# Kernel tuning notes

Hardware: AMD Instinct MI355X
Metric: run time of the kernel (lower is better)

The kernel has to match this reference:

```python
import jax, jax.numpy as jnp
import numpy as np

EMBED_DIM = 1024
BATCH, SEQ = 4, 2048


def setup_inputs() -> dict:
    key = jax.random.key(0)
    k1, k2 = jax.random.split(key)
    hidden_states = jax.random.normal(k1, (BATCH, SEQ, EMBED_DIM), dtype=jnp.float32)
    # fused QKV projection weight (Linear(embed_dim, 3*embed_dim, bias=False)),
    # stored as [E, 3E] so y = x @ W
    W_qkv = jax.random.normal(k2, (EMBED_DIM, 3 * EMBED_DIM), dtype=jnp.float32) * (1.0 / np.sqrt(EMBED_DIM))
    return {"hidden_states": hidden_states, "W_qkv": W_qkv}


def reference(hidden_states, W_qkv):
    E = hidden_states.shape[-1]
    scale = 1.0 / np.sqrt(E)
    qkv = jnp.einsum('bse,ef->bsf', hidden_states, W_qkv)  # [B,S,3E]
    q, k, v = jnp.split(qkv, 3, axis=-1)                   # each [B,S,E]
    # scores = q @ (k^T * scale); softmax over keys
    scores = jnp.einsum('bqe,bke->bqk', q, k) * scale      # [B,S,S]
    w = jax.nn.softmax(scores, axis=-1)
    return jnp.einsum('bqk,bke->bqe', w, v)                # [B,S,E]
```

## Files before the change

### kernel.cpp

```cpp
#include <hip/hip_runtime.h>

typedef __attribute__((ext_vector_type(8))) short short8;
typedef __attribute__((ext_vector_type(8))) unsigned short ushort8;
typedef __attribute__((ext_vector_type(4))) float f32x4;

__device__ __forceinline__ float bf2f(unsigned short u) {
  union { unsigned int u; float f; } c; c.u = ((unsigned int)u) << 16; return c.f;
}
__device__ __forceinline__ unsigned short f2bf(float f) {
  union { float f; unsigned int u; } c; c.f = f;
  unsigned int x = c.u;
  return (unsigned short)((x + 0x7FFFu + ((x >> 16) & 1u)) >> 16);
}

#define GLD_LDS16(g, l)                                                        \
  __builtin_amdgcn_global_load_lds(                                            \
      (const __attribute__((address_space(1))) void*)(g),                      \
      (__attribute__((address_space(3))) void*)(l), 16, 0, 0)

__global__ __launch_bounds__(256) void prep_kernel(
    const float* __restrict__ X, unsigned short* __restrict__ Xb,
    const float* __restrict__ W, unsigned short* __restrict__ Wt) {
  const int t = threadIdx.x;
  if (blockIdx.x < 4096) {
    long i = ((long)blockIdx.x * 256 + t) * 8;
    float4 a = *(const float4*)(X + i);
    float4 b = *(const float4*)(X + i + 4);
    ushort8 o;
    o[0] = f2bf(a.x); o[1] = f2bf(a.y); o[2] = f2bf(a.z); o[3] = f2bf(a.w);
    o[4] = f2bf(b.x); o[5] = f2bf(b.y); o[6] = f2bf(b.z); o[7] = f2bf(b.w);
    *(ushort8*)(Xb + i) = o;
  } else {
    const int bid = blockIdx.x - 4096;
    const int f0 = (bid % 48) * 64;
    const int e0 = (bid / 48) * 64;
    __shared__ unsigned short tile[64][65];
    const int cg = (t & 15) * 4;
    const int r = t >> 4;
#pragma unroll
    for (int i = 0; i < 4; ++i) {
      int e = r + i * 16;
      float4 v = *(const float4*)(W + (long)(e0 + e) * 3072 + f0 + cg);
      tile[e][cg + 0] = f2bf(v.x);
      tile[e][cg + 1] = f2bf(v.y);
      tile[e][cg + 2] = f2bf(v.z);
      tile[e][cg + 3] = f2bf(v.w);
    }
    __syncthreads();
#pragma unroll
    for (int i = 0; i < 4; ++i) {
      int f = (t >> 4) + i * 16;
      int e = (t & 15) * 4;
      ushort4 o;
      o.x = tile[e + 0][f];
      o.y = tile[e + 1][f];
      o.z = tile[e + 2][f];
      o.w = tile[e + 3][f];
      *(ushort4*)(Wt + (long)(f0 + f) * 1024 + e0 + e) = o;
    }
  }
}

template <int MODE>
__device__ __forceinline__ void gemm_body(
    const unsigned short* __restrict__ A, const unsigned short* __restrict__ B,
    void* __restrict__ Cv, int K, int lda, int ldb, int ldc,
    long sA, long sB, long sC, float alpha, float* __restrict__ Lrow,
    unsigned short* __restrict__ Vt) {
  constexpr int BM = 128, BN = 128, BK = 64;
  __shared__ __align__(16) unsigned short smem[BM * BK + BN * BK];
  unsigned short* As = smem;
  unsigned short* Bs = smem + BM * BK;

  const int t = threadIdx.x;
  const int lane = t & 63;
  const int wave = t >> 6;
  const int quad = lane >> 4;
  const int mrow = lane & 15;
  const int wm = wave >> 1, wn = wave & 1;

  const int bx = blockIdx.x, by = blockIdx.y;
  const int rowA0 = by * BM;
  const int rowB0 = bx * BN;
  const int b = blockIdx.z;
  const unsigned short* Ab = A + (long)b * sA;
  const unsigned short* Bb = B + (long)b * sB;

  f32x4 acc[4][4];
#pragma unroll
  for (int i = 0; i < 4; ++i)
#pragma unroll
    for (int j = 0; j < 4; ++j) {
      f32x4 z = {0.f, 0.f, 0.f, 0.f};
      acc[i][j] = z;
    }

  const int rbase = wave * 32 + (lane >> 3);
  const int c2 = lane & 7;

  for (int kt = 0; kt < K; kt += BK) {
#pragma unroll
    for (int j = 0; j < 4; ++j) {
      int r = rbase + j * 8;
      int c = c2 ^ (r & 7);
      GLD_LDS16(Ab + (long)(rowA0 + r) * lda + kt + c * 8, As + (wave * 4 + j) * 512);
      GLD_LDS16(Bb + (long)(rowB0 + r) * ldb + kt + c * 8, Bs + (wave * 4 + j) * 512);
    }
    __syncthreads();
#pragma unroll
    for (int ks = 0; ks < 2; ++ks) {
      short8 af[4], bfr[4];
#pragma unroll
      for (int i = 0; i < 4; ++i) {
        int rA = wm * 64 + i * 16 + mrow;
        int cc = ks * 4 + quad;
        af[i] = *(const short8*)(As + (rA * 8 + (cc ^ (rA & 7))) * 8);
        int rB = wn * 64 + i * 16 + mrow;
        bfr[i] = *(const short8*)(Bs + (rB * 8 + (cc ^ (rB & 7))) * 8);
      }
#pragma unroll
      for (int mt = 0; mt < 4; ++mt)
#pragma unroll
        for (int nt = 0; nt < 4; ++nt)
          acc[mt][nt] = __builtin_amdgcn_mfma_f32_16x16x32_bf16(
              af[mt], bfr[nt], acc[mt][nt], 0, 0, 0);
    }
    __syncthreads();
  }

  const int m_base = rowA0 + wm * 64;
  const int n_base = rowB0 + wn * 64;
  const long cb = (long)b * sC;

  if constexpr (MODE == 0) {
    if (bx < 16) {
#pragma unroll
      for (int mt = 0; mt < 4; ++mt)
#pragma unroll
        for (int nt = 0; nt < 4; ++nt)
#pragma unroll
          for (int i = 0; i < 4; ++i) {
            int row = m_base + mt * 16 + quad * 4 + i;
            int col = n_base + nt * 16 + mrow;
            ((unsigned short*)Cv)[cb + (long)row * ldc + col] = f2bf(acc[mt][nt][i]);
          }
    } else {
#pragma unroll
      for (int mt = 0; mt < 4; ++mt)
#pragma unroll
        for (int nt = 0; nt < 4; ++nt)
#pragma unroll
          for (int i = 0; i < 4; ++i) {
            int r = wm * 64 + mt * 16 + quad * 4 + i;
            int cL = wn * 64 + nt * 16 + mrow;
            int swz = ((cL & 7) << 4) ^ (((cL >> 3) & 3) << 3);
            smem[cL * 128 + (r ^ swz)] = f2bf(acc[mt][nt][i]);
          }
      __syncthreads();
      const int batch = by >> 4;
      const int s_base = (by & 15) * 128;
      const int e_base = (bx - 16) * 128;
      unsigned short* VtB = Vt + (long)batch * 1024 * 2048;
#pragma unroll
      for (int rnd = 0; rnd < 8; ++rnd) {
        int e = (t >> 4) + rnd * 16;
        int s = (t & 15) * 8;
        int swz = ((e & 7) << 4) ^ (((e >> 3) & 3) << 3);
        ushort8 v = *(const ushort8*)(smem + e * 128 + (s ^ swz));
        *(ushort8*)(VtB + (long)(e_base + e) * 2048 + s_base + s) = v;
      }
    }
  } else if constexpr (MODE == 1) {
    float p[4][4];
#pragma unroll
    for (int mt = 0; mt < 4; ++mt)
#pragma unroll
      for (int i = 0; i < 4; ++i) p[mt][i] = 0.f;
#pragma unroll
    for (int mt = 0; mt < 4; ++mt)
#pragma unroll
      for (int nt = 0; nt < 4; ++nt)
#pragma unroll
        for (int i = 0; i < 4; ++i) {
          int row = m_base + mt * 16 + quad * 4 + i;
          int col = n_base + nt * 16 + mrow;
          float e = __expf(acc[mt][nt][i] * alpha);
          ((unsigned short*)Cv)[cb + (long)row * ldc + col] = f2bf(e);
          p[mt][i] += e;
        }
#pragma unroll
    for (int off = 1; off < 16; off <<= 1)
#pragma unroll
      for (int mt = 0; mt < 4; ++mt)
#pragma unroll
        for (int i = 0; i < 4; ++i)
          p[mt][i] += __shfl_xor(p[mt][i], off, 64);
    if (mrow == 0) {
#pragma unroll
      for (int mt = 0; mt < 4; ++mt)
#pragma unroll
        for (int i = 0; i < 4; ++i) {
          int row = m_base + mt * 16 + quad * 4 + i;
          atomicAdd(&Lrow[b * 2048 + row], p[mt][i]);
        }
    }
  } else {
#pragma unroll
    for (int mt = 0; mt < 4; ++mt)
#pragma unroll
      for (int i = 0; i < 4; ++i) {
        int row = m_base + mt * 16 + quad * 4 + i;
        float inv = 1.0f / Lrow[b * 2048 + row];
#pragma unroll
        for (int nt = 0; nt < 4; ++nt) {
          int col = n_base + nt * 16 + mrow;
          ((float*)Cv)[cb + (long)row * ldc + col] = acc[mt][nt][i] * inv;
        }
      }
  }
}

__global__ __launch_bounds__(256, 2) void qkv_gemm_kernel(
    const unsigned short* __restrict__ A, const unsigned short* __restrict__ B,
    void* __restrict__ Cv, int K, int lda, int ldb, int ldc,
    long sA, long sB, long sC, float alpha, float* __restrict__ Lrow,
    unsigned short* __restrict__ Vt) {
  gemm_body<0>(A, B, Cv, K, lda, ldb, ldc, sA, sB, sC, alpha, Lrow, Vt);
}
__global__ __launch_bounds__(256, 2) void score_gemm_kernel(
    const unsigned short* __restrict__ A, const unsigned short* __restrict__ B,
    void* __restrict__ Cv, int K, int lda, int ldb, int ldc,
    long sA, long sB, long sC, float alpha, float* __restrict__ Lrow,
    unsigned short* __restrict__ Vt) {
  gemm_body<1>(A, B, Cv, K, lda, ldb, ldc, sA, sB, sC, alpha, Lrow, Vt);
}
__global__ __launch_bounds__(256, 2) void out_gemm_kernel(
    const unsigned short* __restrict__ A, const unsigned short* __restrict__ B,
    void* __restrict__ Cv, int K, int lda, int ldb, int ldc,
    long sA, long sB, long sC, float alpha, float* __restrict__ Lrow,
    unsigned short* __restrict__ Vt) {
  gemm_body<2>(A, B, Cv, K, lda, ldb, ldc, sA, sB, sC, alpha, Lrow, Vt);
}

extern "C" void kernel_launch(void* const* d_in, const int* in_sizes, int n_in,
                              void* d_out, int out_size, void* d_ws, size_t ws_size,
                              hipStream_t stream) {
  const float* X = (const float*)d_in[0];
  const float* W = (const float*)d_in[1];
  float* out = (float*)d_out;

  char* ws = (char*)d_ws;
  unsigned short* Xb  = (unsigned short*)(ws);
  unsigned short* Wtb = (unsigned short*)(ws + 16777216);
  unsigned short* QKV = (unsigned short*)(ws + 23068672);
  unsigned short* Vt  = (unsigned short*)(ws + 73400320);
  unsigned short* Sb  = (unsigned short*)(ws + 90177536);
  float* Lrow = (float*)(ws + 16777216);

  prep_kernel<<<4864, 256, 0, stream>>>(X, Xb, W, Wtb);

  qkv_gemm_kernel<<<dim3(24, 64, 1), 256, 0, stream>>>(
      Xb, Wtb, QKV, 1024, 1024, 1024, 3072, 0L, 0L, 0L, 1.0f, nullptr, Vt);

  hipMemsetAsync(Lrow, 0, 4 * 2048 * sizeof(float), stream);

  score_gemm_kernel<<<dim3(16, 16, 4), 256, 0, stream>>>(
      QKV, QKV + 1024, Sb, 1024, 3072, 3072, 2048,
      (long)2048 * 3072, (long)2048 * 3072, (long)2048 * 2048, 0.03125f, Lrow, nullptr);

  out_gemm_kernel<<<dim3(8, 16, 4), 256, 0, stream>>>(
      Sb, Vt, out, 2048, 2048, 2048, 1024,
      (long)2048 * 2048, (long)1024 * 2048, (long)2048 * 1024, 1.0f, Lrow, nullptr);
}
```

Baseline: 232.3 us.

## Split-K the output GEMM with atomics, fold memsets into prep, compact QK buffer

Splits the P·V output GEMM along K into two halves, doubling the grid to 1024 blocks, with partial results accumulated into the output by float atomicAdd. The output and the row-sum buffer are now zeroed by extra blocks in the prep kernel, which replaces the separate memset. The QKV projection now stores only Q and K, with a row stride of 2048, because V already goes to the transposed buffer. The V-transpose store to shared memory packs four bf16 values into one ushort4 write. The aim is better occupancy on the output GEMM and one fewer launch, at the cost of atomic traffic on the output and nondeterministic summation order.

```diff
diff --git a/kernel.cpp b/kernel.cpp
--- a/kernel.cpp
+++ b/kernel.cpp
@@ -20,7 +20,8 @@
 
 __global__ __launch_bounds__(256) void prep_kernel(
     const float* __restrict__ X, unsigned short* __restrict__ Xb,
-    const float* __restrict__ W, unsigned short* __restrict__ Wt) {
+    const float* __restrict__ W, unsigned short* __restrict__ Wt,
+    float* __restrict__ out, float* __restrict__ Lrow) {
   const int t = threadIdx.x;
   if (blockIdx.x < 4096) {
     long i = ((long)blockIdx.x * 256 + t) * 8;
@@ -30,7 +31,7 @@
     o[0] = f2bf(a.x); o[1] = f2bf(a.y); o[2] = f2bf(a.z); o[3] = f2bf(a.w);
     o[4] = f2bf(b.x); o[5] = f2bf(b.y); o[6] = f2bf(b.z); o[7] = f2bf(b.w);
     *(ushort8*)(Xb + i) = o;
-  } else {
+  } else if (blockIdx.x < 4864) {
     const int bid = blockIdx.x - 4096;
     const int f0 = (bid % 48) * 64;
     const int e0 = (bid / 48) * 64;
@@ -58,6 +59,15 @@
       o.w = tile[e + 3][f];
       *(ushort4*)(Wt + (long)(f0 + f) * 1024 + e0 + e) = o;
     }
+  } else if (blockIdx.x < 8960) {
+    long base = (long)(blockIdx.x - 4864) * 2048 + t * 8;
+    float4 z = {0.f, 0.f, 0.f, 0.f};
+    *(float4*)(out + base) = z;
+    *(float4*)(out + base + 4) = z;
+  } else {
+    float4 z = {0.f, 0.f, 0.f, 0.f};
+#pragma unroll
+    for (int j = 0; j < 8; ++j) *(float4*)(Lrow + (j * 256 + t) * 4) = z;
   }
 }
 
@@ -82,9 +92,16 @@
   const int bx = blockIdx.x, by = blockIdx.y;
   const int rowA0 = by * BM;
   const int rowB0 = bx * BN;
-  const int b = blockIdx.z;
-  const unsigned short* Ab = A + (long)b * sA;
-  const unsigned short* Bb = B + (long)b * sB;
+  int b, kbase;
+  if constexpr (MODE == 2) {
+    b = blockIdx.z >> 1;
+    kbase = (blockIdx.z & 1) * K;
+  } else {
+    b = blockIdx.z;
+    kbase = 0;
+  }
+  const unsigned short* Ab = A + (long)b * sA + kbase;
+  const unsigned short* Bb = B + (long)b * sB + kbase;
 
   f32x4 acc[4][4];
 #pragma unroll
@@ -148,14 +165,17 @@
 #pragma unroll
       for (int mt = 0; mt < 4; ++mt)
 #pragma unroll
-        for (int nt = 0; nt < 4; ++nt)
-#pragma unroll
-          for (int i = 0; i < 4; ++i) {
-            int r = wm * 64 + mt * 16 + quad * 4 + i;
-            int cL = wn * 64 + nt * 16 + mrow;
-            int swz = ((cL & 7) << 4) ^ (((cL >> 3) & 3) << 3);
-            smem[cL * 128 + (r ^ swz)] = f2bf(acc[mt][nt][i]);
-          }
+        for (int nt = 0; nt < 4; ++nt) {
+          int r4 = wm * 64 + mt * 16 + quad * 4;
+          int cL = wn * 64 + nt * 16 + mrow;
+          int swz = ((cL & 7) << 4) ^ (((cL >> 3) & 3) << 3);
+          ushort4 pk;
+          pk.x = f2bf(acc[mt][nt][0]);
+          pk.y = f2bf(acc[mt][nt][1]);
+          pk.z = f2bf(acc[mt][nt][2]);
+          pk.w = f2bf(acc[mt][nt][3]);
+          *(ushort4*)(smem + cL * 128 + (r4 ^ swz)) = pk;
+        }
       __syncthreads();
       const int batch = by >> 4;
       const int s_base = (by & 15) * 128;
@@ -214,7 +234,7 @@
 #pragma unroll
         for (int nt = 0; nt < 4; ++nt) {
           int col = n_base + nt * 16 + mrow;
-          ((float*)Cv)[cb + (long)row * ldc + col] = acc[mt][nt][i] * inv;
+          atomicAdd((float*)Cv + cb + (long)row * ldc + col, acc[mt][nt][i] * inv);
         }
       }
   }
@@ -252,23 +272,21 @@
   char* ws = (char*)d_ws;
   unsigned short* Xb  = (unsigned short*)(ws);
   unsigned short* Wtb = (unsigned short*)(ws + 16777216);
-  unsigned short* QKV = (unsigned short*)(ws + 23068672);
-  unsigned short* Vt  = (unsigned short*)(ws + 73400320);
-  unsigned short* Sb  = (unsigned short*)(ws + 90177536);
-  float* Lrow = (float*)(ws + 16777216);
-
-  prep_kernel<<<4864, 256, 0, stream>>>(X, Xb, W, Wtb);
+  unsigned short* QK  = (unsigned short*)(ws + 23068672);
+  unsigned short* Vt  = (unsigned short*)(ws + 56623104);
+  unsigned short* Sb  = (unsigned short*)(ws + 73400320);
+  float* Lrow         = (float*)(ws + 106954752);
+
+  prep_kernel<<<8961, 256, 0, stream>>>(X, Xb, W, Wtb, out, Lrow);
 
   qkv_gemm_kernel<<<dim3(24, 64, 1), 256, 0, stream>>>(
-      Xb, Wtb, QKV, 1024, 1024, 1024, 3072, 0L, 0L, 0L, 1.0f, nullptr, Vt);
-
-  hipMemsetAsync(Lrow, 0, 4 * 2048 * sizeof(float), stream);
+      Xb, Wtb, QK, 1024, 1024, 1024, 2048, 0L, 0L, 0L, 1.0f, nullptr, Vt);
 
   score_gemm_kernel<<<dim3(16, 16, 4), 256, 0, stream>>>(
-      QKV, QKV + 1024, Sb, 1024, 3072, 3072, 2048,
-      (long)2048 * 3072, (long)2048 * 3072, (long)2048 * 2048, 0.03125f, Lrow, nullptr);
-
-  out_gemm_kernel<<<dim3(8, 16, 4), 256, 0, stream>>>(
-      Sb, Vt, out, 2048, 2048, 2048, 1024,
+      QK, QK + 1024, Sb, 1024, 2048, 2048, 2048,
+      (long)2048 * 2048, (long)2048 * 2048, (long)2048 * 2048, 0.03125f, Lrow, nullptr);
+
+  out_gemm_kernel<<<dim3(8, 16, 8), 256, 0, stream>>>(
+      Sb, Vt, out, 1024, 2048, 2048, 1024,
       (long)2048 * 2048, (long)1024 * 2048, (long)2048 * 1024, 1.0f, Lrow, nullptr);
 }
```

Result: slower. 265.3 us (+14.2%).
